# Kernel tuning notes

Measured on AMD Instinct MI355X. Metric: run time of the kernel, lower is better.

The kernel has to match this reference:

```python
import jax, jax.numpy as jnp
import numpy as np

SIG_LEVEL = 2
N_UNITS = 1024
INPUT_SIZE = 512
SIGSIZE = sum(2 ** k for k in range(1, SIG_LEVEL + 1))  # siglength(2, L) = 2^(L+1)-2 = 6
SAVED_LEN = N_UNITS * (1 + SIGSIZE)  # 7168
BATCH = 4096


def sigjoin(prev_sigs, disp, time_lapse, level):
    """Chen's identity: new_sig = prev_sig (tensor-mult) exp(v), truncated at `level`.

    prev_sigs: [N, SIGSIZE] flat signature levels (level k occupies 2^k entries),
    disp: [N, 1] displacement in dim 0; dim 1 displacement fixed to time_lapse.
    """
    N = prev_sigs.shape[0]
    v = jnp.concatenate([disp, jnp.full_like(disp, 1.0) * time_lapse], axis=1)  # [N, 2]
    # signature of the straight segment: seg_k = v^{(x)k} / k!
    seg = [v]
    for k in range(2, level + 1):
        seg.append((seg[-1][:, :, None] * v[:, None, :]).reshape(N, -1) / k)
    # split prev signature into levels
    S, off = [], 0
    for k in range(1, level + 1):
        sz = 2 ** k
        S.append(prev_sigs[:, off:off + sz])
        off += sz
    # result_k = S_k + seg_k + sum_{i=1}^{k-1} S_i (x) seg_{k-i}
    out = []
    for k in range(1, level + 1):
        r = S[k - 1] + seg[k - 1]
        for i in range(1, k):
            r = r + (S[i - 1][:, :, None] * seg[k - i - 1][:, None, :]).reshape(N, 2 ** k)
        out.append(r)
    return jnp.concatenate(out, axis=1)


def setup_inputs() -> dict:
    key = jax.random.key(0)
    ks = jax.random.split(key, 8)
    x = jax.random.normal(ks[0], (BATCH, INPUT_SIZE), dtype=jnp.float32)
    prev_sigs = jax.random.normal(ks[1], (BATCH, N_UNITS * SIGSIZE), dtype=jnp.float32) * 0.1
    prev_states = jax.random.normal(ks[2], (BATCH, N_UNITS), dtype=jnp.float32)
    W_w = jax.random.normal(ks[3], (N_UNITS, INPUT_SIZE), dtype=jnp.float32) / np.sqrt(INPUT_SIZE)
    W_b = jax.random.normal(ks[4], (N_UNITS,), dtype=jnp.float32) * 0.01
    U_w = jax.random.normal(ks[5], (N_UNITS, SAVED_LEN), dtype=jnp.float32) / np.sqrt(SAVED_LEN)
    U_b = jax.random.normal(ks[6], (N_UNITS,), dtype=jnp.float32) * 0.01
    log_timelapse = jnp.array([np.log(0.1)], dtype=jnp.float32)
    return {"x": x, "prev_sigs": prev_sigs, "prev_states": prev_states,
            "W_w": W_w, "W_b": W_b, "U_w": U_w, "U_b": U_b,
            "log_timelapse": log_timelapse}


def reference(x, prev_sigs, prev_states, W_w, W_b, U_w, U_b, log_timelapse):
    h = x @ W_w.T + W_b                                  # [B, n_units]
    mem = jnp.concatenate([prev_sigs, prev_states], 1)   # [B, saved_len]
    raw = h + mem @ U_w.T + U_b                          # [B, n_units]
    disp = (raw - prev_states).reshape(-1, 1)            # [B*n_units, 1]
    tl = jnp.exp(log_timelapse)[0]
    sigs = sigjoin(prev_sigs.reshape(-1, SIGSIZE), disp, tl, SIG_LEVEL)
    sigs = sigs.reshape(-1, N_UNITS * SIGSIZE)
    # output_signatures=True: output = [sigs, raw_output]
    return jnp.concatenate([sigs, raw], axis=1)          # [B, n_units*(sigsize+1)]
```

## Files before the change

kernel.cpp:

```cpp
#include <hip/hip_runtime.h>
#include <hip/hip_bf16.h>
#include <cmath>

#define BATCH   4096
#define NUNITS  1024
#define INSIZE  512
#define SIGSZ   6
#define KSIG    (NUNITS * SIGSZ)
#define SAVED   (KSIG + NUNITS)
#define KTOT    (INSIZE + KSIG + NUNITS)
#define OUTW    (NUNITS * (SIGSZ + 1))
#define NKT     (KTOT / 64)

#define WS_AX 0LL
#define WS_AS 2097152LL
#define WS_AT 27262976LL
#define WS_BW 31457280LL
#define WS_BU 31981568LL
#define WS_ELEMS 39321600LL
#define WS_BYTES (WS_ELEMS * 2)

typedef __attribute__((ext_vector_type(8))) short bf16x8;
typedef __attribute__((ext_vector_type(8))) unsigned short u16x8;
typedef __attribute__((ext_vector_type(4))) float f32x4;

__device__ __forceinline__ unsigned short f2bf(float f) {
    union { float f; unsigned int u; } c; c.f = f;
    unsigned int u = c.u;
    return (unsigned short)((u + 0x7FFFu + ((u >> 16) & 1u)) >> 16);
}
__device__ __forceinline__ float bf2f(unsigned short h) {
    union { unsigned int u; float f; } c; c.u = ((unsigned int)h) << 16;
    return c.f;
}

__device__ __forceinline__ int swz(int row, int bytecol) {
    return row * 64 + (((bytecol) ^ ((row & 7) << 4)) >> 1);
}

__global__ __launch_bounds__(256)
void prepack(const float* __restrict__ x, const float* __restrict__ sigs,
             const float* __restrict__ states, const float* __restrict__ Ww,
             const float* __restrict__ Uw, unsigned short* __restrict__ ws)
{
    const long long stride = (long long)gridDim.x * blockDim.x;
    for (long long p = (long long)blockIdx.x * blockDim.x + threadIdx.x;
         p < 4915200LL; p += stride) {
        const float* src; unsigned short* dst; long long o;
        if (p < 262144LL)       { src = x;      dst = ws + WS_AX; o = p; }
        else if (p < 3407872LL) { src = sigs;   dst = ws + WS_AS; o = p - 262144LL; }
        else if (p < 3932160LL) { src = states; dst = ws + WS_AT; o = p - 3407872LL; }
        else if (p < 3997696LL) { src = Ww;     dst = ws + WS_BW; o = p - 3932160LL; }
        else                    { src = Uw;     dst = ws + WS_BU; o = p - 3997696LL; }
        const f32x4 v0 = __builtin_nontemporal_load((const f32x4*)(src + o * 8));
        const f32x4 v1 = __builtin_nontemporal_load((const f32x4*)(src + o * 8) + 1);
        u16x8 h;
        h[0] = f2bf(v0[0]); h[1] = f2bf(v0[1]); h[2] = f2bf(v0[2]); h[3] = f2bf(v0[3]);
        h[4] = f2bf(v1[0]); h[5] = f2bf(v1[1]); h[6] = f2bf(v1[2]); h[7] = f2bf(v1[3]);
        *(u16x8*)(dst + o * 8) = h;
    }
}

#define GLD_LDS(G, L) __builtin_amdgcn_global_load_lds(                        \
        (const __attribute__((address_space(1))) unsigned int*)(G),           \
        (__attribute__((address_space(3))) unsigned int*)(L), 16, 0, 0)

__global__ __launch_bounds__(1024, 1)
void rsig_gemm(const unsigned short* __restrict__ ws,
               const float* __restrict__ Wb,
               const float* __restrict__ Ub,
               const float* __restrict__ lt,
               float* __restrict__ out)
{
    __shared__ unsigned short lds[3 * 16384 + 16384];

    const int t  = threadIdx.x;
    const int bn = blockIdx.x & 7;
    const int bm = blockIdx.x >> 3;

    const int lane = t & 63;
    const int w    = t >> 6;
    const int wm   = w >> 3;
    const int wn   = (w >> 1) & 3;
    const int wk   = w & 1;
    const int lr   = lane & 15;
    const int lg   = lane >> 4;

    const unsigned short* wsAx = ws + WS_AX;
    const unsigned short* wsAs = ws + WS_AS;
    const unsigned short* wsAt = ws + WS_AT;
    const unsigned short* wsBw = ws + WS_BW;
    const unsigned short* wsBu = ws + WS_BU;

    unsigned short* stash = &lds[3 * 16384];
    const int kt0 = 104 + bn * 2;

    const int sRow = lane >> 3;
    const int sCol = 8 * ((lane & 7) ^ sRow);

    f32x4 acc[4][2];
#pragma unroll
    for (int m = 0; m < 4; ++m)
#pragma unroll
        for (int n = 0; n < 2; ++n)
            acc[m][n] = (f32x4)0.f;

#define STAGE(BUF, KT)                                                                  \
    {                                                                                   \
        const int kt_ = (KT);                                                           \
        const unsigned short* abase; int astr, koff;                                    \
        if (kt_ < 8)        { abase = wsAx; astr = INSIZE; koff = kt_ * 64; }           \
        else if (kt_ < 104) { abase = wsAs; astr = KSIG;   koff = kt_ * 64 - 512; }     \
        else                { abase = wsAt; astr = NUNITS; koff = kt_ * 64 - 6656; }    \
        const unsigned short* bbase; int bstr, koffb;                                   \
        if (kt_ < 8)        { bbase = wsBw; bstr = INSIZE; koffb = kt_ * 64; }          \
        else                { bbase = wsBu; bstr = SAVED;  koffb = kt_ * 64 - 512; }    \
        unsigned short* base = &lds[(BUF) * 16384];                                     \
        const unsigned short* ga = abase                                                \
            + (size_t)(bm * 128 + w * 8 + sRow) * astr + koff + sCol;                   \
        GLD_LDS(ga, base + w * 512);                                                    \
        const unsigned short* gb = bbase                                                \
            + (size_t)(bn * 128 + w * 8 + sRow) * bstr + koffb + sCol;                  \
        GLD_LDS(gb, base + 8192 + w * 512);                                             \
    }

    STAGE(0, 0);
    STAGE(1, 1);

    int cur = 0;
    for (int kt = 0; kt < NKT; ++kt) {
        if (kt < NKT - 1) { asm volatile("s_waitcnt vmcnt(2)" ::: "memory"); }
        else              { asm volatile("s_waitcnt vmcnt(0)" ::: "memory"); }
        __builtin_amdgcn_s_barrier();
        __builtin_amdgcn_sched_barrier(0);

        if (kt + 2 < NKT) {
            int nb = cur + 2; if (nb >= 3) nb -= 3;
            STAGE(nb, kt + 2);
        }

        if (kt == kt0) {
            const u16x8 v = *(const u16x8*)&lds[cur * 16384 + t * 8];
            *(u16x8*)&stash[t * 8] = v;
        } else if (kt == kt0 + 1) {
            const u16x8 v = *(const u16x8*)&lds[cur * 16384 + t * 8];
            *(u16x8*)&stash[8192 + t * 8] = v;
        }

        {
            const unsigned short* aT = &lds[cur * 16384];
            const unsigned short* bT = aT + 8192;
            bf16x8 af[4], bfr[2];
#pragma unroll
            for (int m = 0; m < 4; ++m)
                af[m] = *(const bf16x8*)&aT[swz(wm * 64 + m * 16 + lr, wk * 64 + lg * 16)];
#pragma unroll
            for (int n = 0; n < 2; ++n)
                bfr[n] = *(const bf16x8*)&bT[swz(wn * 32 + n * 16 + lr, wk * 64 + lg * 16)];
#pragma unroll
            for (int m = 0; m < 4; ++m)
#pragma unroll
                for (int n = 0; n < 2; ++n)
                    acc[m][n] = __builtin_amdgcn_mfma_f32_16x16x32_bf16(af[m], bfr[n], acc[m][n], 0, 0, 0);
        }

        cur = (cur == 2) ? 0 : cur + 1;
    }

    __syncthreads();

    float* rawt = (float*)lds;
    if (wk == 0) {
#pragma unroll
        for (int n = 0; n < 2; ++n) {
            const int cc = wn * 32 + n * 16 + lr;
            const int ug = bn * 128 + cc;
            const float bias = Wb[ug] + Ub[ug];
#pragma unroll
            for (int m = 0; m < 4; ++m) {
                const int rr = wm * 64 + m * 16 + lg * 4;
#pragma unroll
                for (int i = 0; i < 4; ++i)
                    rawt[(rr + i) * 132 + cc] = acc[m][n][i] + bias;
            }
        }
    }
    __syncthreads();
    if (wk == 1) {
#pragma unroll
        for (int n = 0; n < 2; ++n) {
            const int cc = wn * 32 + n * 16 + lr;
#pragma unroll
            for (int m = 0; m < 4; ++m) {
                const int rr = wm * 64 + m * 16 + lg * 4;
#pragma unroll
                for (int i = 0; i < 4; ++i)
                    rawt[(rr + i) * 132 + cc] += acc[m][n][i];
            }
        }
    }
    __syncthreads();

    const float tl = expf(lt[0]);
    const int r0 = t >> 8;
    const int c  = t & 255;

#define PS(R, CC) bf2f(stash[((CC) >> 6) * 8192 + ((R) >> 3) * 512 + ((R) & 7) * 64 \
                            + (((((CC) & 63) >> 3) ^ ((R) & 7)) << 3) + ((CC) & 7)])

    for (int pass = 0; pass < 32; ++pass) {
        const int r = pass * 4 + r0;
        const long long b = (long long)bm * 128 + r;
        if (c < 192) {
            const int u  = (2 * c) / 3;
            const int cs = c % 3;
            const unsigned short* srow = wsAs + b * KSIG + bn * 768;
            const ushort4 sin = *(const ushort4*)(srow + c * 4);
            const float e0 = bf2f(sin.x), e1 = bf2f(sin.y);
            const float e2 = bf2f(sin.z), e3 = bf2f(sin.w);
            float4 o;
            if (cs == 0) {
                const float d = rawt[r * 132 + u] - PS(r, u);
                o.x = e0 + d;
                o.y = e1 + tl;
                o.z = e2 + d  * (0.5f * d  + e0);
                o.w = e3 + tl * (0.5f * d  + e0);
            } else if (cs == 1) {
                const float d  = rawt[r * 132 + u]     - PS(r, u);
                const float dn = rawt[r * 132 + u + 1] - PS(r, u + 1);
                const float s1 = bf2f(srow[u * 6 + 1]);
                o.x = e0 + d  * (0.5f * tl + s1);
                o.y = e1 + tl * (0.5f * tl + s1);
                o.z = e2 + dn;
                o.w = e3 + tl;
            } else {
                const float d = rawt[r * 132 + u] - PS(r, u);
                const unsigned int sv = *(const unsigned int*)(srow + u * 6);
                const float s0 = bf2f((unsigned short)(sv & 0xffffu));
                const float s1 = bf2f((unsigned short)(sv >> 16));
                o.x = e0 + d  * (0.5f * d  + s0);
                o.y = e1 + tl * (0.5f * d  + s0);
                o.z = e2 + d  * (0.5f * tl + s1);
                o.w = e3 + tl * (0.5f * tl + s1);
            }
            *(float4*)(out + b * OUTW + bn * 768 + c * 4) = o;
        } else if (c < 224) {
            const int cc = (c - 192) * 4;
            const float4 rv = *(const float4*)&rawt[r * 132 + cc];
            *(float4*)(out + b * OUTW + KSIG + bn * 128 + cc) = rv;
        }
    }
#undef PS
#undef STAGE
}

extern "C" void kernel_launch(void* const* d_in, const int* in_sizes, int n_in,
                              void* d_out, int out_size, void* d_ws, size_t ws_size,
                              hipStream_t stream) {
    const float* x      = (const float*)d_in[0];
    const float* sigs   = (const float*)d_in[1];
    const float* states = (const float*)d_in[2];
    const float* Ww     = (const float*)d_in[3];
    const float* Wb     = (const float*)d_in[4];
    const float* Uw     = (const float*)d_in[5];
    const float* Ub     = (const float*)d_in[6];
    const float* lt     = (const float*)d_in[7];
    float* out = (float*)d_out;

    unsigned short* ws = (unsigned short*)d_ws;
    hipLaunchKernelGGL(prepack, dim3(2048), dim3(256), 0, stream,
                       x, sigs, states, Ww, Uw, ws);
    hipLaunchKernelGGL(rsig_gemm, dim3(256), dim3(1024), 0, stream,
                       ws, Wb, Ub, lt, out);
}
```

Before: 147.4 us.

## Fuse bf16 prepack into GEMM kernel with chunked cross-block flag gating

Removes the separate prepack launch. Each of the 256 GEMM blocks converts its share of each 512-wide K chunk to bf16 in the workspace and publishes it through agent-scope atomic counters. Before staging a chunk, a block spins until all blocks have signalled that chunk, so conversion overlaps the GEMM main loop. To free a wave for the conversion work, wave 15 no longer issues loads and wave 14 issues its loads as well. A timeout fallback makes a block convert the whole chunk itself, and the old two-kernel path is kept when the workspace is too small for the flags. The costs are spin-wait latency, a grid-wide dependency that assumes all 256 blocks are co-resident, and extra barriers inside the main loop.

Result: slower. 447.7 us (+203.8%).

```diff
diff --git a/kernel.cpp b/kernel.cpp
--- a/kernel.cpp
+++ b/kernel.cpp
@@ -18,11 +18,14 @@
 #define WS_BW 31457280LL
 #define WS_BU 31981568LL
 #define WS_ELEMS 39321600LL
-#define WS_BYTES (WS_ELEMS * 2)
+#define WS_BYTES (WS_ELEMS * 2LL)
+#define NPREP 256
+#define SPIN_MAX (1LL << 16)
 
 typedef __attribute__((ext_vector_type(8))) short bf16x8;
 typedef __attribute__((ext_vector_type(8))) unsigned short u16x8;
 typedef __attribute__((ext_vector_type(4))) float f32x4;
+typedef __attribute__((ext_vector_type(2))) float f32x2;
 
 __device__ __forceinline__ unsigned short f2bf(float f) {
     union { float f; unsigned int u; } c; c.f = f;
@@ -36,6 +39,41 @@
 
 __device__ __forceinline__ int swz(int row, int bytecol) {
     return row * 64 + (((bytecol) ^ ((row & 7) << 4)) >> 1);
+}
+
+__device__ __forceinline__ void cvt_share(int c, int pb, int t,
+    const float* __restrict__ x, const float* __restrict__ sigs,
+    const float* __restrict__ states, const float* __restrict__ Ww,
+    const float* __restrict__ Uw, unsigned short* __restrict__ wsm)
+{
+#pragma unroll
+    for (int k8 = 0; k8 < 8; ++k8) {
+        const int kt = c * 8 + k8;
+        if (t < 512) {
+            const int g   = pb * 512 + t;
+            const int row = g >> 5;
+            const int cp  = (g & 31) * 2;
+            const float* src; unsigned short* dst; int str, koff;
+            if (kt < 8)        { src = x;      dst = wsm + WS_AX; str = INSIZE; koff = kt * 64; }
+            else if (kt < 104) { src = sigs;   dst = wsm + WS_AS; str = KSIG;   koff = kt * 64 - 512; }
+            else               { src = states; dst = wsm + WS_AT; str = NUNITS; koff = kt * 64 - 6656; }
+            const f32x2 v = __builtin_nontemporal_load(
+                (const f32x2*)(src + (size_t)row * str + koff + cp));
+            *(unsigned int*)(dst + (size_t)row * str + koff + cp) =
+                (unsigned int)f2bf(v[0]) | ((unsigned int)f2bf(v[1]) << 16);
+        } else if (t < 640) {
+            const int g2  = pb * 128 + (t - 512);
+            const int row = g2 >> 5;
+            const int cp  = (g2 & 31) * 2;
+            const float* src; unsigned short* dst; int str, koff;
+            if (kt < 8) { src = Ww; dst = wsm + WS_BW; str = INSIZE; koff = kt * 64; }
+            else        { src = Uw; dst = wsm + WS_BU; str = SAVED;  koff = kt * 64 - 512; }
+            const f32x2 v = __builtin_nontemporal_load(
+                (const f32x2*)(src + (size_t)row * str + koff + cp));
+            *(unsigned int*)(dst + (size_t)row * str + koff + cp) =
+                (unsigned int)f2bf(v[0]) | ((unsigned int)f2bf(v[1]) << 16);
+        }
+    }
 }
 
 __global__ __launch_bounds__(256)
@@ -66,17 +104,26 @@
         (__attribute__((address_space(3))) unsigned int*)(L), 16, 0, 0)
 
 __global__ __launch_bounds__(1024, 1)
-void rsig_gemm(const unsigned short* __restrict__ ws,
-               const float* __restrict__ Wb,
-               const float* __restrict__ Ub,
-               const float* __restrict__ lt,
-               float* __restrict__ out)
+void rsig_fused(const unsigned short* __restrict__ ws,
+                const float* __restrict__ Wb,
+                const float* __restrict__ Ub,
+                const float* __restrict__ lt,
+                float* __restrict__ out,
+                const float* __restrict__ x,
+                const float* __restrict__ sigs,
+                const float* __restrict__ states,
+                const float* __restrict__ Ww,
+                const float* __restrict__ Uw,
+                int* __restrict__ flags,
+                const int gated)
 {
     __shared__ unsigned short lds[3 * 16384 + 16384];
-
-    const int t  = threadIdx.x;
-    const int bn = blockIdx.x & 7;
-    const int bm = blockIdx.x >> 3;
+    __shared__ int gateStat;
+
+    const int t   = threadIdx.x;
+    const int bid = blockIdx.x;
+    const int bn  = bid & 7;
+    const int bm  = bid >> 3;
 
     const int lane = t & 63;
     const int w    = t >> 6;
@@ -91,6 +138,7 @@
     const unsigned short* wsAt = ws + WS_AT;
     const unsigned short* wsBw = ws + WS_BW;
     const unsigned short* wsBu = ws + WS_BU;
+    unsigned short* wsm = (unsigned short*)ws;
 
     unsigned short* stash = &lds[3 * 16384];
     const int kt0 = 104 + bn * 2;
@@ -105,7 +153,7 @@
         for (int n = 0; n < 2; ++n)
             acc[m][n] = (f32x4)0.f;
 
-#define STAGE(BUF, KT)                                                                  \
+#define STAGE1(BUF, KT, G)                                                              \
     {                                                                                   \
         const int kt_ = (KT);                                                           \
         const unsigned short* abase; int astr, koff;                                    \
@@ -117,26 +165,77 @@
         else                { bbase = wsBu; bstr = SAVED;  koffb = kt_ * 64 - 512; }    \
         unsigned short* base = &lds[(BUF) * 16384];                                     \
         const unsigned short* ga = abase                                                \
-            + (size_t)(bm * 128 + w * 8 + sRow) * astr + koff + sCol;                   \
-        GLD_LDS(ga, base + w * 512);                                                    \
+            + (size_t)(bm * 128 + (G) * 8 + sRow) * astr + koff + sCol;                 \
+        GLD_LDS(ga, base + (G) * 512);                                                  \
         const unsigned short* gb = bbase                                                \
-            + (size_t)(bn * 128 + w * 8 + sRow) * bstr + koffb + sCol;                  \
-        GLD_LDS(gb, base + 8192 + w * 512);                                             \
-    }
-
+            + (size_t)(bn * 128 + (G) * 8 + sRow) * bstr + koffb + sCol;                \
+        GLD_LDS(gb, base + 8192 + (G) * 512);                                           \
+    }
+#define STAGE(BUF, KT)                                                                  \
+    {                                                                                   \
+        if (w < 14)       { STAGE1(BUF, KT, w); }                                       \
+        else if (w == 14) { STAGE1(BUF, KT, 14); STAGE1(BUF, KT, 15); }                 \
+    }
+#define GATE(M)                                                                         \
+    {                                                                                   \
+        if (w == 15 && lane == 0) {                                                     \
+            int ok = 0;                                                                 \
+            for (long long it_ = 0; it_ < SPIN_MAX; ++it_) {                            \
+                if (__hip_atomic_load(&flags[M], __ATOMIC_ACQUIRE,                      \
+                                      __HIP_MEMORY_SCOPE_AGENT) >= NPREP) { ok = 1; break; } \
+                __builtin_amdgcn_s_sleep(8);                                            \
+            }                                                                           \
+            gateStat = ok;                                                              \
+        }                                                                               \
+        __syncthreads();                                                                \
+        if (!gateStat) {                                                                \
+            for (int p_ = 0; p_ < NPREP; ++p_)                                          \
+                cvt_share((M), p_, t, x, sigs, states, Ww, Uw, wsm);                    \
+            __syncthreads();                                                            \
+        }                                                                               \
+    }
+
+    if (gated) {
+        cvt_share(0, bid, t, x, sigs, states, Ww, Uw, wsm);
+        cvt_share(1, bid, t, x, sigs, states, Ww, Uw, wsm);
+        __syncthreads();
+        if (t == 0) {
+            __threadfence();
+            __hip_atomic_fetch_add(&flags[0], 1, __ATOMIC_RELEASE, __HIP_MEMORY_SCOPE_AGENT);
+            __hip_atomic_fetch_add(&flags[1], 1, __ATOMIC_RELEASE, __HIP_MEMORY_SCOPE_AGENT);
+        }
+        GATE(0);
+    }
     STAGE(0, 0);
     STAGE(1, 1);
 
     int cur = 0;
     for (int kt = 0; kt < NKT; ++kt) {
-        if (kt < NKT - 1) { asm volatile("s_waitcnt vmcnt(2)" ::: "memory"); }
-        else              { asm volatile("s_waitcnt vmcnt(0)" ::: "memory"); }
+        const int st = kt + 2;
+        if (gated && st < NKT && (st & 7) == 0) GATE(st >> 3);
+
+        if (kt < NKT - 1) {
+            if (w < 14)       { asm volatile("s_waitcnt vmcnt(2)" ::: "memory"); }
+            else if (w == 14) { asm volatile("s_waitcnt vmcnt(4)" ::: "memory"); }
+        } else {
+            asm volatile("s_waitcnt vmcnt(0)" ::: "memory");
+        }
         __builtin_amdgcn_s_barrier();
         __builtin_amdgcn_sched_barrier(0);
 
-        if (kt + 2 < NKT) {
+        if (gated && (kt & 7) == 0 && (kt >> 3) + 2 <= 14) {
+            const int cc = (kt >> 3) + 2;
+            cvt_share(cc, bid, t, x, sigs, states, Ww, Uw, wsm);
+            __syncthreads();
+            if (t == 0) {
+                __threadfence();
+                __hip_atomic_fetch_add(&flags[cc], 1, __ATOMIC_RELEASE, __HIP_MEMORY_SCOPE_AGENT);
+            }
+        }
+
+        if (st < NKT) {
             int nb = cur + 2; if (nb >= 3) nb -= 3;
-            STAGE(nb, kt + 2);
+            STAGE(nb, st);
         }
 
         if (kt == kt0) {
@@ -252,6 +351,8 @@
     }
 #undef PS
 #undef STAGE
+#undef STAGE1
+#undef GATE
 }
 
 extern "C" void kernel_launch(void* const* d_in, const int* in_sizes, int n_in,
@@ -268,8 +369,17 @@
     float* out = (float*)d_out;
 
     unsigned short* ws = (unsigned short*)d_ws;
-    hipLaunchKernelGGL(prepack, dim3(2048), dim3(256), 0, stream,
-                       x, sigs, states, Ww, Uw, ws);
-    hipLaunchKernelGGL(rsig_gemm, dim3(256), dim3(1024), 0, stream,
-                       ws, Wb, Ub, lt, out);
-}
+    int* flags = (int*)((char*)d_ws + WS_BYTES);
+    const bool fits = ws_size >= (size_t)WS_BYTES + 64;
+
+    if (fits) {
+        hipMemsetAsync(flags, 0, 64, stream);
+        hipLaunchKernelGGL(rsig_fused, dim3(256), dim3(1024), 0, stream,
+                           ws, Wb, Ub, lt, out, x, sigs, states, Ww, Uw, flags, 1);
+    } else {
+        hipLaunchKernelGGL(prepack, dim3(2048), dim3(256), 0, stream,
+                           x, sigs, states, Ww, Uw, ws);
+        hipLaunchKernelGGL(rsig_fused, dim3(256), dim3(1024), 0, stream,
+                           ws, Wb, Ub, lt, out, x, sigs, states, Ww, Uw, (int*)d_ws, 0);
+    }
+}
```
